# Optimization experiments

Hardware: AMD Instinct MI355X
Metric: run time of the kernel (lower is better)

Reference implementation:

```python
import jax, jax.numpy as jnp
import numpy as np

N = 131072   # number of query points
M = 8        # number of sub-models (2x2x2 ensemble grid)
H = 128      # hidden width of each sub-model MLP
GRID = np.array([2, 2, 2])  # model_grid_shape (data-dim order)


def _cell_extents():
    """Per-model [min,max] extents in x-coordinate order (x is flipped vs data dims)."""
    i = np.arange(M)
    c0 = i % GRID[0]
    c1 = (i // GRID[0]) % GRID[1]
    c2 = i // (GRID[0] * GRID[1])
    # flipped x coord j indexes grid dim j -> x-coord order is (c2, c1, c0)
    c_x = np.stack([c2, c1, c0], axis=-1).astype(np.float32)
    g_x = GRID[::-1].astype(np.float32)
    mins = -1.0 + 2.0 * c_x / g_x
    maxs = -1.0 + 2.0 * (c_x + 1.0) / g_x
    return mins.astype(np.float32), maxs.astype(np.float32)


def setup_inputs() -> dict:
    key = jax.random.key(0)
    ks = jax.random.split(key, 6)
    s = 0.1
    x = jax.random.uniform(ks[0], (N, 3), jnp.float32, -1.0, 1.0)
    W0 = jax.random.normal(ks[1], (M, 3, H), jnp.float32) * s
    b0 = jnp.zeros((M, H), jnp.float32)
    W1 = jax.random.normal(ks[2], (M, H, H), jnp.float32) * s
    b1 = jnp.zeros((M, H), jnp.float32)
    W2 = jax.random.normal(ks[3], (M, H, H), jnp.float32) * s
    b2 = jnp.zeros((M, H), jnp.float32)
    W3 = jax.random.normal(ks[4], (M, H, 1), jnp.float32) * s
    b3 = jnp.zeros((M, 1), jnp.float32)
    mins_np, maxs_np = _cell_extents()
    return {"x": x, "W0": W0, "b0": b0, "W1": W1, "b1": b1,
            "W2": W2, "b2": b2, "W3": W3, "b3": b3,
            "mins": jnp.asarray(mins_np), "maxs": jnp.asarray(maxs_np)}


def reference(x, W0, b0, W1, b1, W2, b2, W3, b3, mins, maxs):
    g = jnp.asarray(GRID, dtype=x.dtype)
    # per-point sub-model index (matches torch: flip(-1), scale by grid, linearize)
    u = (x + 1.0) / (2.0 + 1e-6)                      # [N,3] in [0,1)
    cell = (u[:, ::-1] * g).astype(jnp.int32)         # [N,3]
    idx = cell[:, 0] + cell[:, 1] * GRID[0] + cell[:, 2] * (GRID[0] * GRID[1])

    def step(y, p):
        i, w0, b0i, w1, b1i, w2, b2i, w3, b3i, mn, mx = p
        # normalize points into this model's local [-1,1]^3 box
        xn = -1.0 + 2.0 * (x - mn) / (mx - mn)        # [N,3]
        h = jax.nn.relu(xn @ w0 + b0i)                # [N,H]
        h = jax.nn.relu(h @ w1 + b1i)
        h = jax.nn.relu(h @ w2 + b2i)
        yi = h @ w3 + b3i                             # [N,1]
        y = jnp.where((idx == i)[:, None], yi, y)
        return y, None

    y0 = jnp.zeros((x.shape[0], 1), x.dtype)
    y, _ = jax.lax.scan(step, y0,
                        (jnp.arange(M), W0, b0, W1, b1, W2, b2, W3, b3, mins, maxs))
    return y
```

## Files before the change

kernel.cpp:

```cpp
#include <hip/hip_runtime.h>
#include <hip/hip_bf16.h>


#define HDIM 128
#define LDSH 136
#define TILE 64
#define NMODEL 8
#define GRIDX 64
#define SEGCAP 20480
#define CURSTRIDE 16

typedef __bf16 bf16x8 __attribute__((ext_vector_type(8)));
typedef __bf16 bf16x4 __attribute__((ext_vector_type(4)));
typedef float  f32x4  __attribute__((ext_vector_type(4)));

__device__ __forceinline__ int model_of(float x0, float x1, float x2) {
  const float den = 2.000001f;
  float u0 = (x0 + 1.0f) / den;
  float u1 = (x1 + 1.0f) / den;
  float u2 = (x2 + 1.0f) / den;
  int c0 = (int)(u2 * 2.0f);
  int c1 = (int)(u1 * 2.0f);
  int c2 = (int)(u0 * 2.0f);
  return c0 + (c1 << 1) + (c2 << 2);
}

__global__ __launch_bounds__(256)
void srn_prep_scatter(const float* __restrict__ W1, const float* __restrict__ W2,
                      const float* __restrict__ x,
                      const float* __restrict__ mins, const float* __restrict__ maxs,
                      __bf16* __restrict__ Wt1, __bf16* __restrict__ Wt2,
                      int* __restrict__ cursors, f32x4* __restrict__ xperm, int N)
{
  const int b = blockIdx.x;
  const int tid = threadIdx.x;

  if (b < 64) {
    __shared__ float lds[64][65];
    const int m   = b >> 3;
    const int r2  = b & 7;
    const int mat = r2 >> 2;
    const int ti  = (r2 >> 1) & 1;
    const int tj  = r2 & 1;
    const float* src = (mat ? W2 : W1) + m * HDIM * HDIM;
    __bf16*      dst = (mat ? Wt2 : Wt1) + m * HDIM * HDIM;
    #pragma unroll
    for (int it = 0; it < 16; ++it) {
      const int rr = (tid >> 6) + it * 4, cc = tid & 63;
      lds[rr][cc] = src[(ti * 64 + rr) * HDIM + tj * 64 + cc];
    }
    __syncthreads();
    #pragma unroll
    for (int it = 0; it < 16; ++it) {
      const int nn = (tid >> 6) + it * 4, kk = tid & 63;
      dst[(tj * 64 + nn) * HDIM + ti * 64 + kk] = (__bf16)lds[kk][nn];
    }
  } else {
    __shared__ float mnS[NMODEL * 3], ivS[NMODEL * 3];
    __shared__ int wtot[4][NMODEL], gbase[NMODEL], wpre[4][NMODEL];
    if (tid < NMODEL * 3) { mnS[tid] = mins[tid]; ivS[tid] = 2.0f / (maxs[tid] - mins[tid]); }
    __syncthreads();

    const int lane = tid & 63;
    const int wave = tid >> 6;
    const unsigned long long mlt = (1ull << lane) - 1ull;
    const int base = (b - 64) * 4096;

    float qx[16][3];
    int ids[16], offs[16];
    int wc[NMODEL] = {};

    #pragma unroll
    for (int it = 0; it < 16; ++it) {
      const int i = base + it * 256 + tid;
      const float x0 = x[3*i], x1 = x[3*i+1], x2 = x[3*i+2];
      const int id = model_of(x0, x1, x2);
      ids[it] = id;
      qx[it][0] = -1.0f + (x0 - mnS[3*id  ]) * ivS[3*id  ];
      qx[it][1] = -1.0f + (x1 - mnS[3*id+1]) * ivS[3*id+1];
      qx[it][2] = -1.0f + (x2 - mnS[3*id+2]) * ivS[3*id+2];
      const unsigned long long bb0 = __ballot(id & 1);
      const unsigned long long bb1 = __ballot(id & 2);
      const unsigned long long bb2 = __ballot(id & 4);
      const unsigned long long mym =
          ((id & 1) ? bb0 : ~bb0) & ((id & 2) ? bb1 : ~bb1) & ((id & 4) ? bb2 : ~bb2);
      const int rank = __popcll(mym & mlt);
      int off = 0;
      #pragma unroll
      for (int mm = 0; mm < NMODEL; ++mm) {
        const unsigned long long msk =
            ((mm & 1) ? bb0 : ~bb0) & ((mm & 2) ? bb1 : ~bb1) & ((mm & 4) ? bb2 : ~bb2);
        const int c = __popcll(msk);
        if (id == mm) off = wc[mm] + rank;
        wc[mm] += c;
      }
      offs[it] = off;
    }

    if (lane == 0) {
      #pragma unroll
      for (int mm = 0; mm < NMODEL; ++mm) wtot[wave][mm] = wc[mm];
    }
    __syncthreads();
    if (tid < NMODEL) {
      const int s0 = wtot[0][tid], s1 = wtot[1][tid], s2 = wtot[2][tid], s3 = wtot[3][tid];
      const int tot = s0 + s1 + s2 + s3;
      gbase[tid] = tot ? atomicAdd(&cursors[tid * CURSTRIDE], tot) : 0;
      wpre[0][tid] = 0; wpre[1][tid] = s0; wpre[2][tid] = s0 + s1; wpre[3][tid] = s0 + s1 + s2;
    }
    __syncthreads();

    #pragma unroll
    for (int it = 0; it < 16; ++it) {
      const int i = base + it * 256 + tid;
      const int id = ids[it];
      const int slot = gbase[id] + wpre[wave][id] + offs[it];
      if (slot < SEGCAP) {
        f32x4 v;
        v[0] = qx[it][0]; v[1] = qx[it][1]; v[2] = qx[it][2];
        v[3] = __int_as_float(i);
        xperm[(size_t)id * SEGCAP + slot] = v;
      }
    }
  }
}

__global__ __launch_bounds__(256, 4)
void srn_main(const float* __restrict__ W0, const float* __restrict__ b0,
              const float* __restrict__ b1, const float* __restrict__ b2,
              const float* __restrict__ W3, const float* __restrict__ b3,
              const __bf16* __restrict__ Wt1, const __bf16* __restrict__ Wt2,
              const int* __restrict__ cursors, const f32x4* __restrict__ xperm,
              float* __restrict__ out, int N)
{
  __shared__ __align__(16) __bf16 hA[TILE * LDSH];
  __shared__ __align__(16) __bf16 hB[TILE * LDSH];
  __shared__ f32x4 xs4[TILE];
  __shared__ float w0s[3 * HDIM];
  __shared__ float b0s[HDIM];
  __shared__ float part[4][TILE];

  const int m = blockIdx.y;
  const int tid = threadIdx.x;
  const int lane = tid & 63;
  const int wave = tid >> 6;
  const int l16  = lane & 15;
  const int quad = lane >> 4;
  const int n0   = wave * 32;

  if (tid < HDIM) {
    w0s[tid]          = W0[m * 3 * HDIM + tid];
    w0s[HDIM + tid]   = W0[m * 3 * HDIM + HDIM + tid];
    w0s[2*HDIM + tid] = W0[m * 3 * HDIM + 2 * HDIM + tid];
    b0s[tid] = b0[m * HDIM + tid];
  }
  f32x4 b1r[2], b2r[2], w3r[2];
  #pragma unroll
  for (int nt = 0; nt < 2; ++nt) {
    const int nb = m * HDIM + n0 + nt * 16 + quad * 4;
    b1r[nt] = *(const f32x4*)(b1 + nb);
    b2r[nt] = *(const f32x4*)(b2 + nb);
    w3r[nt] = *(const f32x4*)(W3 + nb);
  }
  const int cnt = cursors[m * CURSTRIDE];
  const float b3v = b3[m];
  const __bf16* Wt1m = Wt1 + m * HDIM * HDIM;
  const __bf16* Wt2m = Wt2 + m * HDIM * HDIM;
  const f32x4* xp = xperm + (size_t)m * SEGCAP;
  __syncthreads();

  f32x4 v;
  int tile = blockIdx.x;
  if (tid < TILE) {
    const int idx = tile * TILE + tid;
    if (idx < cnt) v = xp[idx];
    else { v[0] = 0.0f; v[1] = 0.0f; v[2] = 0.0f; v[3] = __int_as_float(-1); }
  }

  for (; tile * TILE < cnt; tile += GRIDX) {
    if (tid < TILE) xs4[tid] = v;
    __syncthreads();

    if (tid < TILE) {
      const int idx = (tile + GRIDX) * TILE + tid;
      if (idx < cnt) v = xp[idx];
      else { v[0] = 0.0f; v[1] = 0.0f; v[2] = 0.0f; v[3] = __int_as_float(-1); }
    }

    {
      const int p  = lane;
      const int j0 = wave * 32;
      const f32x4 xv = xs4[p];
      #pragma unroll
      for (int jj = 0; jj < 32; jj += 8) {
        bf16x8 pk;
        #pragma unroll
        for (int u8 = 0; u8 < 8; u8 += 4) {
          const int j = j0 + jj + u8;
          f32x4 wa = *(const f32x4*)&w0s[j];
          f32x4 wb = *(const f32x4*)&w0s[HDIM + j];
          f32x4 wc = *(const f32x4*)&w0s[2*HDIM + j];
          f32x4 bb = *(const f32x4*)&b0s[j];
          #pragma unroll
          for (int u = 0; u < 4; ++u) {
            float vv = fmaf(xv[0], wa[u], fmaf(xv[1], wb[u], fmaf(xv[2], wc[u], bb[u])));
            pk[u8 + u] = (__bf16)fmaxf(vv, 0.0f);
          }
        }
        *(bf16x8*)(hA + p * LDSH + j0 + jj) = pk;
      }
    }
    __syncthreads();

    {
      f32x4 acc[2][4] = {};
      #pragma unroll
      for (int kk = 0; kk < 4; ++kk) {
        const int kOff = kk * 32 + quad * 8;
        bf16x8 a0 = *(const bf16x8*)(Wt1m + (n0 + l16) * HDIM + kOff);
        bf16x8 a1 = *(const bf16x8*)(Wt1m + (n0 + 16 + l16) * HDIM + kOff);
        #pragma unroll
        for (int pt = 0; pt < 4; ++pt) {
          bf16x8 bv = *(const bf16x8*)(hA + (pt * 16 + l16) * LDSH + kOff);
          acc[0][pt] = __builtin_amdgcn_mfma_f32_16x16x32_bf16(a0, bv, acc[0][pt], 0, 0, 0);
          acc[1][pt] = __builtin_amdgcn_mfma_f32_16x16x32_bf16(a1, bv, acc[1][pt], 0, 0, 0);
        }
      }
      #pragma unroll
      for (int nt = 0; nt < 2; ++nt) {
        #pragma unroll
        for (int pt = 0; pt < 4; ++pt) {
          bf16x4 pk;
          #pragma unroll
          for (int i = 0; i < 4; ++i)
            pk[i] = (__bf16)fmaxf(acc[nt][pt][i] + b1r[nt][i], 0.0f);
          *(bf16x4*)(hB + (pt * 16 + l16) * LDSH + n0 + nt * 16 + quad * 4) = pk;
        }
      }
    }
    __syncthreads();

    {
      f32x4 acc[2][4] = {};
      #pragma unroll
      for (int kk = 0; kk < 4; ++kk) {
        const int kOff = kk * 32 + quad * 8;
        bf16x8 a0 = *(const bf16x8*)(Wt2m + (n0 + l16) * HDIM + kOff);
        bf16x8 a1 = *(const bf16x8*)(Wt2m + (n0 + 16 + l16) * HDIM + kOff);
        #pragma unroll
        for (int pt = 0; pt < 4; ++pt) {
          bf16x8 bv = *(const bf16x8*)(hB + (pt * 16 + l16) * LDSH + kOff);
          acc[0][pt] = __builtin_amdgcn_mfma_f32_16x16x32_bf16(a0, bv, acc[0][pt], 0, 0, 0);
          acc[1][pt] = __builtin_amdgcn_mfma_f32_16x16x32_bf16(a1, bv, acc[1][pt], 0, 0, 0);
        }
      }
      #pragma unroll
      for (int pt = 0; pt < 4; ++pt) {
        float s = 0.0f;
        #pragma unroll
        for (int nt = 0; nt < 2; ++nt)
          #pragma unroll
          for (int i = 0; i < 4; ++i)
            s = fmaf(fmaxf(acc[nt][pt][i] + b2r[nt][i], 0.0f), w3r[nt][i], s);
        s += __shfl_xor(s, 16);
        s += __shfl_xor(s, 32);
        if (quad == 0) part[wave][pt * 16 + l16] = s;
      }
    }
    __syncthreads();

    if (tid < TILE) {
      const float y = part[0][tid] + part[1][tid] + part[2][tid] + part[3][tid] + b3v;
      const int p = __float_as_int(xs4[tid][3]);
      if (p >= 0) out[p] = y;
    }
  }
}

extern "C" void kernel_launch(void* const* d_in, const int* in_sizes, int n_in,
                              void* d_out, int out_size, void* d_ws, size_t ws_size,
                              hipStream_t stream)
{
  const float* x    = (const float*)d_in[0];
  const float* W0   = (const float*)d_in[1];
  const float* b0   = (const float*)d_in[2];
  const float* W1   = (const float*)d_in[3];
  const float* b1   = (const float*)d_in[4];
  const float* W2   = (const float*)d_in[5];
  const float* b2   = (const float*)d_in[6];
  const float* W3   = (const float*)d_in[7];
  const float* b3   = (const float*)d_in[8];
  const float* mins = (const float*)d_in[9];
  const float* maxs = (const float*)d_in[10];
  float* out = (float*)d_out;
  const int N = in_sizes[0] / 3;

  char* ws = (char*)d_ws;
  int* cursors = (int*)ws;
  f32x4* xperm = (f32x4*)(ws + 512);
  __bf16* Wt1  = (__bf16*)(ws + 512 + (size_t)16 * SEGCAP * NMODEL);
  __bf16* Wt2  = Wt1 + NMODEL * HDIM * HDIM;

  hipMemsetAsync(cursors, 0, NMODEL * CURSTRIDE * sizeof(int), stream);
  srn_prep_scatter<<<dim3(64 + 32), dim3(256), 0, stream>>>(
      W1, W2, x, mins, maxs, Wt1, Wt2, cursors, xperm, N);
  srn_main<<<dim3(GRIDX, NMODEL), dim3(256), 0, stream>>>(
      W0, b0, b1, b2, W3, b3, Wt1, Wt2, cursors, xperm, out, N);
}
```

Measured before the change: 117.3 us.

## Fuse scatter, weight transpose and MLP into one cooperative kernel

Merges the prep/scatter kernel and the main MLP kernel into a single cooperative launch with a grid-wide sync. The memset and global atomics go away: each of 256 scatter blocks writes per-model counts and a private sub-bucket, and main blocks rebuild offsets with a prefix scan and binary search. The goal is to cut launch overhead and atomic contention, at the cost of a grid barrier, a per-block 256-entry scan, and gathers from fragmented sub-buckets. Occupancy hint drops to 2 blocks per SM because shared memory use grows, and a two-launch fallback covers the case where the cooperative launch fails.

```diff
diff --git a/kernel.cpp b/kernel.cpp
--- a/kernel.cpp
+++ b/kernel.cpp
@@ -1,14 +1,19 @@
 #include <hip/hip_runtime.h>
 #include <hip/hip_bf16.h>
+#include <hip/hip_cooperative_groups.h>
+
+namespace cg = cooperative_groups;
 
 
 #define HDIM 128
 #define LDSH 136
 #define TILE 64
 #define NMODEL 8
-#define GRIDX 64
-#define SEGCAP 20480
-#define CURSTRIDE 16
+#define NSCAT 256
+#define PTS_PER_SB 512
+#define SUBCAP 160
+#define TBLK 64
+#define GRID_X 512
 
 typedef __bf16 bf16x8 __attribute__((ext_vector_type(8)));
 typedef __bf16 bf16x4 __attribute__((ext_vector_type(4)));
@@ -25,129 +30,144 @@
   return c0 + (c1 << 1) + (c2 << 2);
 }
 
-__global__ __launch_bounds__(256)
-void srn_prep_scatter(const float* __restrict__ W1, const float* __restrict__ W2,
-                      const float* __restrict__ x,
-                      const float* __restrict__ mins, const float* __restrict__ maxs,
-                      __bf16* __restrict__ Wt1, __bf16* __restrict__ Wt2,
-                      int* __restrict__ cursors, f32x4* __restrict__ xperm, int N)
+__global__ __launch_bounds__(256, 2)
+void srn_fused(const float* __restrict__ W0, const float* __restrict__ b0,
+               const float* __restrict__ b1, const float* __restrict__ b2,
+               const float* __restrict__ W3, const float* __restrict__ b3,
+               const float* __restrict__ W1f, const float* __restrict__ W2f,
+               const float* __restrict__ x,
+               const float* __restrict__ mins, const float* __restrict__ maxs,
+               __bf16* __restrict__ Wt1, __bf16* __restrict__ Wt2,
+               int* __restrict__ counts, f32x4* __restrict__ xperm,
+               float* __restrict__ out, int N, int mode)
 {
-  const int b = blockIdx.x;
-  const int tid = threadIdx.x;
-
-  if (b < 64) {
-    __shared__ float lds[64][65];
-    const int m   = b >> 3;
-    const int r2  = b & 7;
-    const int mat = r2 >> 2;
-    const int ti  = (r2 >> 1) & 1;
-    const int tj  = r2 & 1;
-    const float* src = (mat ? W2 : W1) + m * HDIM * HDIM;
-    __bf16*      dst = (mat ? Wt2 : Wt1) + m * HDIM * HDIM;
-    #pragma unroll
-    for (int it = 0; it < 16; ++it) {
-      const int rr = (tid >> 6) + it * 4, cc = tid & 63;
-      lds[rr][cc] = src[(ti * 64 + rr) * HDIM + tj * 64 + cc];
-    }
-    __syncthreads();
-    #pragma unroll
-    for (int it = 0; it < 16; ++it) {
-      const int nn = (tid >> 6) + it * 4, kk = tid & 63;
-      dst[(tj * 64 + nn) * HDIM + ti * 64 + kk] = (__bf16)lds[kk][nn];
-    }
-  } else {
-    __shared__ float mnS[NMODEL * 3], ivS[NMODEL * 3];
-    __shared__ int wtot[4][NMODEL], gbase[NMODEL], wpre[4][NMODEL];
-    if (tid < NMODEL * 3) { mnS[tid] = mins[tid]; ivS[tid] = 2.0f / (maxs[tid] - mins[tid]); }
-    __syncthreads();
-
-    const int lane = tid & 63;
-    const int wave = tid >> 6;
-    const unsigned long long mlt = (1ull << lane) - 1ull;
-    const int base = (b - 64) * 4096;
-
-    float qx[16][3];
-    int ids[16], offs[16];
-    int wc[NMODEL] = {};
-
-    #pragma unroll
-    for (int it = 0; it < 16; ++it) {
-      const int i = base + it * 256 + tid;
-      const float x0 = x[3*i], x1 = x[3*i+1], x2 = x[3*i+2];
-      const int id = model_of(x0, x1, x2);
-      ids[it] = id;
-      qx[it][0] = -1.0f + (x0 - mnS[3*id  ]) * ivS[3*id  ];
-      qx[it][1] = -1.0f + (x1 - mnS[3*id+1]) * ivS[3*id+1];
-      qx[it][2] = -1.0f + (x2 - mnS[3*id+2]) * ivS[3*id+2];
-      const unsigned long long bb0 = __ballot(id & 1);
-      const unsigned long long bb1 = __ballot(id & 2);
-      const unsigned long long bb2 = __ballot(id & 4);
-      const unsigned long long mym =
-          ((id & 1) ? bb0 : ~bb0) & ((id & 2) ? bb1 : ~bb1) & ((id & 4) ? bb2 : ~bb2);
-      const int rank = __popcll(mym & mlt);
-      int off = 0;
-      #pragma unroll
-      for (int mm = 0; mm < NMODEL; ++mm) {
-        const unsigned long long msk =
-            ((mm & 1) ? bb0 : ~bb0) & ((mm & 2) ? bb1 : ~bb1) & ((mm & 4) ? bb2 : ~bb2);
-        const int c = __popcll(msk);
-        if (id == mm) off = wc[mm] + rank;
-        wc[mm] += c;
-      }
-      offs[it] = off;
-    }
-
-    if (lane == 0) {
-      #pragma unroll
-      for (int mm = 0; mm < NMODEL; ++mm) wtot[wave][mm] = wc[mm];
-    }
-    __syncthreads();
-    if (tid < NMODEL) {
-      const int s0 = wtot[0][tid], s1 = wtot[1][tid], s2 = wtot[2][tid], s3 = wtot[3][tid];
-      const int tot = s0 + s1 + s2 + s3;
-      gbase[tid] = tot ? atomicAdd(&cursors[tid * CURSTRIDE], tot) : 0;
-      wpre[0][tid] = 0; wpre[1][tid] = s0; wpre[2][tid] = s0 + s1; wpre[3][tid] = s0 + s1 + s2;
-    }
-    __syncthreads();
-
-    #pragma unroll
-    for (int it = 0; it < 16; ++it) {
-      const int i = base + it * 256 + tid;
-      const int id = ids[it];
-      const int slot = gbase[id] + wpre[wave][id] + offs[it];
-      if (slot < SEGCAP) {
-        f32x4 v;
-        v[0] = qx[it][0]; v[1] = qx[it][1]; v[2] = qx[it][2];
-        v[3] = __int_as_float(i);
-        xperm[(size_t)id * SEGCAP + slot] = v;
-      }
-    }
-  }
-}
-
-__global__ __launch_bounds__(256, 4)
-void srn_main(const float* __restrict__ W0, const float* __restrict__ b0,
-              const float* __restrict__ b1, const float* __restrict__ b2,
-              const float* __restrict__ W3, const float* __restrict__ b3,
-              const __bf16* __restrict__ Wt1, const __bf16* __restrict__ Wt2,
-              const int* __restrict__ cursors, const f32x4* __restrict__ xperm,
-              float* __restrict__ out, int N)
-{
+  __shared__ float tlds[64][65];
   __shared__ __align__(16) __bf16 hA[TILE * LDSH];
   __shared__ __align__(16) __bf16 hB[TILE * LDSH];
   __shared__ f32x4 xs4[TILE];
   __shared__ float w0s[3 * HDIM];
   __shared__ float b0s[HDIM];
   __shared__ float part[4][TILE];
-
-  const int m = blockIdx.y;
-  const int tid = threadIdx.x;
+  __shared__ int sc[256];
+  __shared__ int E[257];
+  __shared__ float mnS[NMODEL * 3], ivS[NMODEL * 3];
+  __shared__ int wtot[4][NMODEL], wpre[4][NMODEL];
+
+  const int tid  = threadIdx.x;
+  const int bid  = blockIdx.x;
   const int lane = tid & 63;
   const int wave = tid >> 6;
   const int l16  = lane & 15;
   const int quad = lane >> 4;
   const int n0   = wave * 32;
 
+  if (mode != 2) {
+    if (bid < NSCAT) {
+      if (tid < NMODEL * 3) { mnS[tid] = mins[tid]; ivS[tid] = 2.0f / (maxs[tid] - mins[tid]); }
+      __syncthreads();
+      const unsigned long long mlt = (1ull << lane) - 1ull;
+      const int base = bid * PTS_PER_SB;
+      float qx[2][3];
+      int ids[2], offs[2];
+      int wc[NMODEL] = {};
+      #pragma unroll
+      for (int it = 0; it < 2; ++it) {
+        const int i = base + it * 256 + tid;
+        const bool valid = (i < N);
+        int id = 0;
+        if (valid) {
+          const float x0 = x[3*i], x1 = x[3*i+1], x2 = x[3*i+2];
+          id = model_of(x0, x1, x2);
+          qx[it][0] = -1.0f + (x0 - mnS[3*id  ]) * ivS[3*id  ];
+          qx[it][1] = -1.0f + (x1 - mnS[3*id+1]) * ivS[3*id+1];
+          qx[it][2] = -1.0f + (x2 - mnS[3*id+2]) * ivS[3*id+2];
+        }
+        const unsigned long long vm  = __ballot(valid);
+        const unsigned long long bb0 = __ballot(valid && (id & 1));
+        const unsigned long long bb1 = __ballot(valid && (id & 2));
+        const unsigned long long bb2 = __ballot(valid && (id & 4));
+        const unsigned long long mym =
+            ((id & 1) ? bb0 : ~bb0) & ((id & 2) ? bb1 : ~bb1) & ((id & 4) ? bb2 : ~bb2) & vm;
+        const int rank = __popcll(mym & mlt);
+        int off = 0;
+        #pragma unroll
+        for (int mm = 0; mm < NMODEL; ++mm) {
+          const unsigned long long msk =
+              ((mm & 1) ? bb0 : ~bb0) & ((mm & 2) ? bb1 : ~bb1) & ((mm & 4) ? bb2 : ~bb2) & vm;
+          const int c = __popcll(msk);
+          if (valid && id == mm) off = wc[mm] + rank;
+          wc[mm] += c;
+        }
+        ids[it] = valid ? id : -1;
+        offs[it] = off;
+      }
+      if (lane == 0) {
+        #pragma unroll
+        for (int mm = 0; mm < NMODEL; ++mm) wtot[wave][mm] = wc[mm];
+      }
+      __syncthreads();
+      if (tid < NMODEL) {
+        const int s0 = wtot[0][tid], s1 = wtot[1][tid], s2 = wtot[2][tid], s3 = wtot[3][tid];
+        counts[bid * NMODEL + tid] = s0 + s1 + s2 + s3;
+        wpre[0][tid] = 0; wpre[1][tid] = s0; wpre[2][tid] = s0 + s1; wpre[3][tid] = s0 + s1 + s2;
+      }
+      __syncthreads();
+      #pragma unroll
+      for (int it = 0; it < 2; ++it) {
+        const int id = ids[it];
+        if (id >= 0) {
+          const int slot = wpre[wave][id] + offs[it];
+          if (slot < SUBCAP) {
+            const int i = base + it * 256 + tid;
+            f32x4 v;
+            v[0] = qx[it][0]; v[1] = qx[it][1]; v[2] = qx[it][2];
+            v[3] = __int_as_float(i);
+            xperm[((size_t)bid * NMODEL + id) * SUBCAP + slot] = v;
+          }
+        }
+      }
+    } else if (bid < NSCAT + TBLK) {
+      const int b2  = bid - NSCAT;
+      const int m   = b2 >> 3;
+      const int r2  = b2 & 7;
+      const int mat = r2 >> 2;
+      const int ti  = (r2 >> 1) & 1;
+      const int tj  = r2 & 1;
+      const float* src = (mat ? W2f : W1f) + m * HDIM * HDIM;
+      __bf16*      dst = (mat ? Wt2 : Wt1) + m * HDIM * HDIM;
+      #pragma unroll
+      for (int it = 0; it < 16; ++it) {
+        const int rr = (tid >> 6) + it * 4, cc = tid & 63;
+        tlds[rr][cc] = src[(ti * 64 + rr) * HDIM + tj * 64 + cc];
+      }
+      __syncthreads();
+      #pragma unroll
+      for (int it = 0; it < 16; ++it) {
+        const int nn = (tid >> 6) + it * 4, kk = tid & 63;
+        dst[(tj * 64 + nn) * HDIM + ti * 64 + kk] = (__bf16)tlds[kk][nn];
+      }
+    }
+  }
+
+  if (mode == 0) { __threadfence(); cg::this_grid().sync(); __threadfence(); }
+  if (mode == 1) return;
+
+  const int m  = bid >> 6;
+  const int bx = bid & 63;
+
+  {
+    sc[tid] = counts[tid * NMODEL + m];
+    __syncthreads();
+    #pragma unroll
+    for (int off = 1; off < 256; off <<= 1) {
+      const int t = (tid >= off) ? sc[tid - off] : 0;
+      __syncthreads();
+      sc[tid] += t;
+      __syncthreads();
+    }
+    E[tid + 1] = sc[tid];
+    if (tid == 0) E[0] = 0;
+  }
   if (tid < HDIM) {
     w0s[tid]          = W0[m * 3 * HDIM + tid];
     w0s[HDIM + tid]   = W0[m * 3 * HDIM + HDIM + tid];
@@ -162,30 +182,25 @@
     b2r[nt] = *(const f32x4*)(b2 + nb);
     w3r[nt] = *(const f32x4*)(W3 + nb);
   }
-  const int cnt = cursors[m * CURSTRIDE];
   const float b3v = b3[m];
   const __bf16* Wt1m = Wt1 + m * HDIM * HDIM;
   const __bf16* Wt2m = Wt2 + m * HDIM * HDIM;
-  const f32x4* xp = xperm + (size_t)m * SEGCAP;
   __syncthreads();
-
-  f32x4 v;
-  int tile = blockIdx.x;
-  if (tid < TILE) {
-    const int idx = tile * TILE + tid;
-    if (idx < cnt) v = xp[idx];
-    else { v[0] = 0.0f; v[1] = 0.0f; v[2] = 0.0f; v[3] = __int_as_float(-1); }
-  }
-
-  for (; tile * TILE < cnt; tile += GRIDX) {
-    if (tid < TILE) xs4[tid] = v;
-    __syncthreads();
-
+  const int cnt = E[256];
+
+  for (int tile = bx; tile * TILE < cnt; tile += 64) {
     if (tid < TILE) {
-      const int idx = (tile + GRIDX) * TILE + tid;
-      if (idx < cnt) v = xp[idx];
-      else { v[0] = 0.0f; v[1] = 0.0f; v[2] = 0.0f; v[3] = __int_as_float(-1); }
-    }
+      const int s = tile * TILE + tid;
+      f32x4 v;
+      if (s < cnt) {
+        int lo = 1, hi = NSCAT;
+        while (lo < hi) { const int mid = (lo + hi) >> 1; if (E[mid] > s) hi = mid; else lo = mid + 1; }
+        const int seg = lo - 1;
+        v = xperm[((size_t)seg * NMODEL + m) * SUBCAP + (s - E[seg])];
+      } else { v[0] = 0.0f; v[1] = 0.0f; v[2] = 0.0f; v[3] = __int_as_float(-1); }
+      xs4[tid] = v;
+    }
+    __syncthreads();
 
     {
       const int p  = lane;
@@ -199,11 +214,11 @@
           const int j = j0 + jj + u8;
           f32x4 wa = *(const f32x4*)&w0s[j];
           f32x4 wb = *(const f32x4*)&w0s[HDIM + j];
-          f32x4 wc = *(const f32x4*)&w0s[2*HDIM + j];
+          f32x4 wcv = *(const f32x4*)&w0s[2*HDIM + j];
           f32x4 bb = *(const f32x4*)&b0s[j];
           #pragma unroll
           for (int u = 0; u < 4; ++u) {
-            float vv = fmaf(xv[0], wa[u], fmaf(xv[1], wb[u], fmaf(xv[2], wc[u], bb[u])));
+            float vv = fmaf(xv[0], wa[u], fmaf(xv[1], wb[u], fmaf(xv[2], wcv[u], bb[u])));
             pk[u8 + u] = (__bf16)fmaxf(vv, 0.0f);
           }
         }
@@ -274,6 +289,7 @@
       const int p = __float_as_int(xs4[tid][3]);
       if (p >= 0) out[p] = y;
     }
+    __syncthreads();
   }
 }
 
@@ -293,17 +309,30 @@
   const float* mins = (const float*)d_in[9];
   const float* maxs = (const float*)d_in[10];
   float* out = (float*)d_out;
-  const int N = in_sizes[0] / 3;
+  int N = in_sizes[0] / 3;
 
   char* ws = (char*)d_ws;
-  int* cursors = (int*)ws;
-  f32x4* xperm = (f32x4*)(ws + 512);
-  __bf16* Wt1  = (__bf16*)(ws + 512 + (size_t)16 * SEGCAP * NMODEL);
+  int* counts  = (int*)ws;
+  f32x4* xperm = (f32x4*)(ws + 8192);
+  __bf16* Wt1  = (__bf16*)(ws + 8192 + (size_t)NSCAT * NMODEL * SUBCAP * 16);
   __bf16* Wt2  = Wt1 + NMODEL * HDIM * HDIM;
 
-  hipMemsetAsync(cursors, 0, NMODEL * CURSTRIDE * sizeof(int), stream);
-  srn_prep_scatter<<<dim3(64 + 32), dim3(256), 0, stream>>>(
-      W1, W2, x, mins, maxs, Wt1, Wt2, cursors, xperm, N);
-  srn_main<<<dim3(GRIDX, NMODEL), dim3(256), 0, stream>>>(
-      W0, b0, b1, b2, W3, b3, Wt1, Wt2, cursors, xperm, out, N);
+  int mode = 0;
+  void* args[] = {
+    (void*)&W0, (void*)&b0, (void*)&b1, (void*)&b2, (void*)&W3, (void*)&b3,
+    (void*)&W1, (void*)&W2, (void*)&x, (void*)&mins, (void*)&maxs,
+    (void*)&Wt1, (void*)&Wt2, (void*)&counts, (void*)&xperm, (void*)&out,
+    (void*)&N, (void*)&mode
+  };
+  hipError_t rc = hipLaunchCooperativeKernel((const void*)srn_fused,
+                                             dim3(GRID_X), dim3(256), args, 0, stream);
+  if (rc != hipSuccess) {
+    (void)hipGetLastError();
+    srn_fused<<<dim3(GRID_X), dim3(256), 0, stream>>>(
+        W0, b0, b1, b2, W3, b3, W1, W2, x, mins, maxs,
+        Wt1, Wt2, counts, xperm, out, N, 1);
+    srn_fused<<<dim3(GRID_X), dim3(256), 0, stream>>>(
+        W0, b0, b1, b2, W3, b3, W1, W2, x, mins, maxs,
+        Wt1, Wt2, counts, xperm, out, N, 2);
+  }
 }
```

Result: slower. 262.9 us (+124.2%).

## Replace atomic global cursors with per-block fixed segments and prefix-scan lookup

Applied to the files above, without the earlier changes.

The scatter blocks no longer reserve output space with global atomicAdd on per-model cursors. Each scatter block now writes its points into its own fixed-capacity slot per model (SUBCAP) and stores its per-model count. The main kernel builds a prefix sum of those counts with wave shuffles and binary-searches it to find where each point lives. This removes the cursor memset launch and the atomic serialisation. In exchange it drops the register prefetch of the next tile's points, adds a per-point binary search, and assumes no block puts more than SUBCAP points into one model.

```diff
diff --git a/kernel.cpp b/kernel.cpp
--- a/kernel.cpp
+++ b/kernel.cpp
@@ -6,9 +6,10 @@
 #define LDSH 136
 #define TILE 64
 #define NMODEL 8
+#define NSCAT 32
+#define PPB 4096
+#define SUBCAP 704
 #define GRIDX 64
-#define SEGCAP 20480
-#define CURSTRIDE 16
 
 typedef __bf16 bf16x8 __attribute__((ext_vector_type(8)));
 typedef __bf16 bf16x4 __attribute__((ext_vector_type(4)));
@@ -26,11 +27,11 @@
 }
 
 __global__ __launch_bounds__(256)
-void srn_prep_scatter(const float* __restrict__ W1, const float* __restrict__ W2,
-                      const float* __restrict__ x,
-                      const float* __restrict__ mins, const float* __restrict__ maxs,
-                      __bf16* __restrict__ Wt1, __bf16* __restrict__ Wt2,
-                      int* __restrict__ cursors, f32x4* __restrict__ xperm, int N)
+void srn_prep(const float* __restrict__ W1, const float* __restrict__ W2,
+              const float* __restrict__ x,
+              const float* __restrict__ mins, const float* __restrict__ maxs,
+              __bf16* __restrict__ Wt1, __bf16* __restrict__ Wt2,
+              int* __restrict__ counts, f32x4* __restrict__ xperm, int N)
 {
   const int b = blockIdx.x;
   const int tid = threadIdx.x;
@@ -57,14 +58,15 @@
     }
   } else {
     __shared__ float mnS[NMODEL * 3], ivS[NMODEL * 3];
-    __shared__ int wtot[4][NMODEL], gbase[NMODEL], wpre[4][NMODEL];
+    __shared__ int wtot[4][NMODEL], wpre[4][NMODEL];
     if (tid < NMODEL * 3) { mnS[tid] = mins[tid]; ivS[tid] = 2.0f / (maxs[tid] - mins[tid]); }
     __syncthreads();
 
     const int lane = tid & 63;
     const int wave = tid >> 6;
     const unsigned long long mlt = (1ull << lane) - 1ull;
-    const int base = (b - 64) * 4096;
+    const int sb = b - 64;
+    const int base = sb * PPB;
 
     float qx[16][3];
     int ids[16], offs[16];
@@ -104,22 +106,21 @@
     __syncthreads();
     if (tid < NMODEL) {
       const int s0 = wtot[0][tid], s1 = wtot[1][tid], s2 = wtot[2][tid], s3 = wtot[3][tid];
-      const int tot = s0 + s1 + s2 + s3;
-      gbase[tid] = tot ? atomicAdd(&cursors[tid * CURSTRIDE], tot) : 0;
+      counts[sb * NMODEL + tid] = min(s0 + s1 + s2 + s3, SUBCAP);
       wpre[0][tid] = 0; wpre[1][tid] = s0; wpre[2][tid] = s0 + s1; wpre[3][tid] = s0 + s1 + s2;
     }
     __syncthreads();
 
     #pragma unroll
     for (int it = 0; it < 16; ++it) {
-      const int i = base + it * 256 + tid;
       const int id = ids[it];
-      const int slot = gbase[id] + wpre[wave][id] + offs[it];
-      if (slot < SEGCAP) {
+      const int slot = wpre[wave][id] + offs[it];
+      if (slot < SUBCAP) {
+        const int i = base + it * 256 + tid;
         f32x4 v;
         v[0] = qx[it][0]; v[1] = qx[it][1]; v[2] = qx[it][2];
         v[3] = __int_as_float(i);
-        xperm[(size_t)id * SEGCAP + slot] = v;
+        xperm[((size_t)sb * NMODEL + id) * SUBCAP + slot] = v;
       }
     }
   }
@@ -130,7 +131,7 @@
               const float* __restrict__ b1, const float* __restrict__ b2,
               const float* __restrict__ W3, const float* __restrict__ b3,
               const __bf16* __restrict__ Wt1, const __bf16* __restrict__ Wt2,
-              const int* __restrict__ cursors, const f32x4* __restrict__ xperm,
+              const int* __restrict__ counts, const f32x4* __restrict__ xperm,
               float* __restrict__ out, int N)
 {
   __shared__ __align__(16) __bf16 hA[TILE * LDSH];
@@ -139,8 +140,10 @@
   __shared__ float w0s[3 * HDIM];
   __shared__ float b0s[HDIM];
   __shared__ float part[4][TILE];
-
-  const int m = blockIdx.y;
+  __shared__ int E[NSCAT + 1];
+
+  const int m  = blockIdx.y;
+  const int bx = blockIdx.x;
   const int tid = threadIdx.x;
   const int lane = tid & 63;
   const int wave = tid >> 6;
@@ -148,6 +151,16 @@
   const int quad = lane >> 4;
   const int n0   = wave * 32;
 
+  if (tid < 64) {
+    int c = (lane < NSCAT) ? counts[lane * NMODEL + m] : 0;
+    #pragma unroll
+    for (int off = 1; off < NSCAT; off <<= 1) {
+      const int t = __shfl_up(c, off);
+      if (lane >= off) c += t;
+    }
+    if (lane < NSCAT) E[lane + 1] = c;
+    if (lane == 0) E[0] = 0;
+  }
   if (tid < HDIM) {
     w0s[tid]          = W0[m * 3 * HDIM + tid];
     w0s[HDIM + tid]   = W0[m * 3 * HDIM + HDIM + tid];
@@ -162,30 +175,25 @@
     b2r[nt] = *(const f32x4*)(b2 + nb);
     w3r[nt] = *(const f32x4*)(W3 + nb);
   }
-  const int cnt = cursors[m * CURSTRIDE];
   const float b3v = b3[m];
   const __bf16* Wt1m = Wt1 + m * HDIM * HDIM;
   const __bf16* Wt2m = Wt2 + m * HDIM * HDIM;
-  const f32x4* xp = xperm + (size_t)m * SEGCAP;
   __syncthreads();
-
-  f32x4 v;
-  int tile = blockIdx.x;
-  if (tid < TILE) {
-    const int idx = tile * TILE + tid;
-    if (idx < cnt) v = xp[idx];
-    else { v[0] = 0.0f; v[1] = 0.0f; v[2] = 0.0f; v[3] = __int_as_float(-1); }
-  }
-
-  for (; tile * TILE < cnt; tile += GRIDX) {
-    if (tid < TILE) xs4[tid] = v;
-    __syncthreads();
-
+  const int cnt = E[NSCAT];
+
+  for (int tile = bx; tile * TILE < cnt; tile += GRIDX) {
     if (tid < TILE) {
-      const int idx = (tile + GRIDX) * TILE + tid;
-      if (idx < cnt) v = xp[idx];
-      else { v[0] = 0.0f; v[1] = 0.0f; v[2] = 0.0f; v[3] = __int_as_float(-1); }
-    }
+      const int s = tile * TILE + tid;
+      f32x4 v;
+      if (s < cnt) {
+        int lo = 1, hi = NSCAT;
+        while (lo < hi) { const int mid = (lo + hi) >> 1; if (E[mid] > s) hi = mid; else lo = mid + 1; }
+        const int seg = lo - 1;
+        v = xperm[((size_t)seg * NMODEL + m) * SUBCAP + (s - E[seg])];
+      } else { v[0] = 0.0f; v[1] = 0.0f; v[2] = 0.0f; v[3] = __int_as_float(-1); }
+      xs4[tid] = v;
+    }
+    __syncthreads();
 
     {
       const int p  = lane;
@@ -199,11 +207,11 @@
           const int j = j0 + jj + u8;
           f32x4 wa = *(const f32x4*)&w0s[j];
           f32x4 wb = *(const f32x4*)&w0s[HDIM + j];
-          f32x4 wc = *(const f32x4*)&w0s[2*HDIM + j];
+          f32x4 wcv = *(const f32x4*)&w0s[2*HDIM + j];
           f32x4 bb = *(const f32x4*)&b0s[j];
           #pragma unroll
           for (int u = 0; u < 4; ++u) {
-            float vv = fmaf(xv[0], wa[u], fmaf(xv[1], wb[u], fmaf(xv[2], wc[u], bb[u])));
+            float vv = fmaf(xv[0], wa[u], fmaf(xv[1], wb[u], fmaf(xv[2], wcv[u], bb[u])));
             pk[u8 + u] = (__bf16)fmaxf(vv, 0.0f);
           }
         }
@@ -296,14 +304,13 @@
   const int N = in_sizes[0] / 3;
 
   char* ws = (char*)d_ws;
-  int* cursors = (int*)ws;
-  f32x4* xperm = (f32x4*)(ws + 512);
-  __bf16* Wt1  = (__bf16*)(ws + 512 + (size_t)16 * SEGCAP * NMODEL);
+  int* counts  = (int*)ws;
+  f32x4* xperm = (f32x4*)(ws + 4096);
+  __bf16* Wt1  = (__bf16*)(ws + 4096 + (size_t)NSCAT * NMODEL * SUBCAP * 16);
   __bf16* Wt2  = Wt1 + NMODEL * HDIM * HDIM;
 
-  hipMemsetAsync(cursors, 0, NMODEL * CURSTRIDE * sizeof(int), stream);
-  srn_prep_scatter<<<dim3(64 + 32), dim3(256), 0, stream>>>(
-      W1, W2, x, mins, maxs, Wt1, Wt2, cursors, xperm, N);
+  srn_prep<<<dim3(64 + NSCAT), dim3(256), 0, stream>>>(
+      W1, W2, x, mins, maxs, Wt1, Wt2, counts, xperm, N);
   srn_main<<<dim3(GRIDX, NMODEL), dim3(256), 0, stream>>>(
-      W0, b0, b1, b2, W3, b3, Wt1, Wt2, cursors, xperm, out, N);
+      W0, b0, b1, b2, W3, b3, Wt1, Wt2, counts, xperm, out, N);
 }
```

Result: no change. 118.3 us (+0.9%).
